# Kernel tuning notes

Measured on AMD Instinct MI355X. Metric: run time of the kernel, lower is better.

Reference implementation:

```python
import jax, jax.numpy as jnp
import numpy as np

NEW_SEQ_LEN = 150  # hard-coded in the original forward


def _interp_one(x, length):
    """PyTorch F.interpolate(mode='linear', align_corners=False) on x[:length].
    x: [T, D] float, length: scalar int. Returns [NEW_SEQ_LEN, D]."""
    lf = length.astype(jnp.float32)
    scale = lf / NEW_SEQ_LEN
    src = (jnp.arange(NEW_SEQ_LEN, dtype=jnp.float32) + 0.5) * scale - 0.5
    src = jnp.maximum(src, 0.0)
    i0 = jnp.floor(src).astype(jnp.int32)
    i0 = jnp.minimum(i0, length - 1)
    i1 = jnp.minimum(i0 + 1, length - 1)
    w = (src - i0.astype(jnp.float32))[:, None]  # [150, 1]
    return x[i0] * (1.0 - w) + x[i1] * w


_interp_batch = jax.vmap(_interp_one)  # ragged per-sample interpolation, fused over batch


def setup_inputs() -> dict:
    key = jax.random.key(0)
    ks = jax.random.split(key, 8)
    B, T, C_IMU, C_EMG, EMB, CSD = 2048, 512, 48, 16, 64, 256
    x_imu = jax.random.normal(ks[0], (B, T, C_IMU), jnp.float32)
    x_emg = jax.random.normal(ks[1], (B, T, C_EMG), jnp.float32)
    lens = jax.random.randint(ks[2], (B,), 160, T + 1, jnp.int32)  # >= NEW_SEQ_LEN
    w_emb_imu = jax.random.normal(ks[3], (C_IMU, EMB), jnp.float32) / np.sqrt(C_IMU)
    b_emb_imu = jnp.zeros((EMB,), jnp.float32)
    w_emb_emg = jax.random.normal(ks[4], (C_EMG, EMB), jnp.float32) / np.sqrt(C_EMG)
    b_emb_emg = jnp.zeros((EMB,), jnp.float32)
    w_proj = jax.random.normal(ks[5], (NEW_SEQ_LEN * EMB, CSD), jnp.float32) / np.sqrt(NEW_SEQ_LEN * EMB)
    b_proj = jnp.zeros((CSD,), jnp.float32)
    return {"x_imu": x_imu, "x_emg": x_emg, "lens": lens,
            "w_emb_imu": w_emb_imu, "b_emb_imu": b_emb_imu,
            "w_emb_emg": w_emb_emg, "b_emb_emg": b_emb_emg,
            "w_proj": w_proj, "b_proj": b_proj}


def reference(x_imu, x_emg, lens, w_emb_imu, b_emb_imu, w_emb_emg, b_emb_emg, w_proj, b_proj):
    B = x_imu.shape[0]
    # embedding nets (per-timestep linear encoders) -> [B, T, 64]
    seq_imu = jnp.einsum('btc,ce->bte', x_imu, w_emb_imu) + b_emb_imu
    seq_emg = jnp.einsum('btc,ce->bte', x_emg, w_emb_emg) + b_emb_emg
    # ragged linear interpolation of each sample's first lens[i] steps to 150
    seq_imu = _interp_batch(seq_imu, lens)  # [B, 150, 64]
    seq_emg = _interp_batch(seq_emg, lens)
    # flatten and project; NOTE: original code applies linear_proj_imu to BOTH
    out_imu = seq_imu.reshape(B, -1) @ w_proj + b_proj
    out_emg = seq_emg.reshape(B, -1) @ w_proj + b_proj
    return (out_imu, out_emg)
```

## Files before the change

### kernel.cpp

```cpp
#include <hip/hip_runtime.h>

#define NEWL 150
#define EMBD 64
#define NCOL 256
#define CIMU 48
#define CEMG 16

#define KIMU (NEWL * CIMU)
#define KEMG (NEWL * CEMG)
#define KSTI 225
#define KSTE 75
#define NCI 5
#define SCH_I 30
#define NG_I 15
#define NG_E 25

typedef __bf16 bf16x8_t __attribute__((ext_vector_type(8)));
typedef __bf16 bf16x4_t __attribute__((ext_vector_type(4)));
typedef float f32x4_t __attribute__((ext_vector_type(4)));

__device__ __forceinline__ f32x4_t mfma16(bf16x8_t a, bf16x8_t b, f32x4_t c) {
  return __builtin_amdgcn_mfma_f32_16x16x32_bf16(a, b, c, 0, 0, 0);
}

template <int C, int KST>
__device__ void wcomb_body(const float* __restrict__ wemb,
                           const float* __restrict__ wreg_src,
                           __bf16* __restrict__ wpk, int s, int j) {
  float wreg[EMBD];
#pragma unroll
  for (int e = 0; e < EMBD; ++e) wreg[e] = wreg_src[(size_t)e * NCOL];
  const int cb = j >> 4, lr = j & 15;
#pragma unroll
  for (int q = 0; q < C / 8; ++q) {
    const int kq = (s * C) / 8 + q;
    const int ks = kq >> 2, h = kq & 3;
    bf16x8_t tv;
#pragma unroll
    for (int u = 0; u < 8; ++u) {
      const float* we = wemb + (q * 8 + u) * EMBD;
      float acc = 0.f;
#pragma unroll
      for (int e = 0; e < EMBD; ++e) acc = fmaf(we[e], wreg[e], acc);
      tv[u] = (__bf16)acc;
    }
    *(bf16x8_t*)(wpk + (((size_t)cb * KST + ks) * 64 + h * 16 + lr) * 8) = tv;
  }
}

__global__ __launch_bounds__(256) void wcomb_kernel(
    const float* __restrict__ w_emb_imu, const float* __restrict__ w_emb_emg,
    const float* __restrict__ b_emb_imu, const float* __restrict__ b_emb_emg,
    const float* __restrict__ w_proj,
    __bf16* __restrict__ wpk_imu, __bf16* __restrict__ wpk_emg,
    float* __restrict__ bpart) {
  const int s = blockIdx.x, m = blockIdx.y, j = threadIdx.x;
  const float* wp_base = w_proj + (size_t)s * EMBD * NCOL + j;
  const float* be = (m == 0) ? b_emb_imu : b_emb_emg;
  float bacc = 0.f;
#pragma unroll
  for (int e = 0; e < EMBD; ++e) bacc = fmaf(be[e], wp_base[(size_t)e * NCOL], bacc);
  bpart[((size_t)m * NEWL + s) * NCOL + j] = bacc;
  if (m == 0)
    wcomb_body<CIMU, KSTI>(w_emb_imu, wp_base, wpk_imu, s, j);
  else
    wcomb_body<CEMG, KSTE>(w_emb_emg, wp_base, wpk_emg, s, j);
}

__global__ __launch_bounds__(256) void fused_kernel(
    const float* __restrict__ x_imu, const float* __restrict__ x_emg,
    const int* __restrict__ lens,
    const __bf16* __restrict__ wpk_imu, const __bf16* __restrict__ wpk_emg,
    const float* __restrict__ b_proj, const float* __restrict__ bpart,
    float* __restrict__ p_imu, float* __restrict__ p_emg,
    float* __restrict__ bias, int B, int T) {
  const int bid = blockIdx.x;
  const int span = B >> 4;
  const int mts = B >> 5;
  if (bid == (NCI + 1) * span) {
    const int j = threadIdx.x;
#pragma unroll
    for (int m = 0; m < 2; ++m) {
      float acc = b_proj[j];
      for (int s = 0; s < NEWL; ++s) acc += bpart[((size_t)m * NEWL + s) * NCOL + j];
      bias[m * NCOL + j] = acc;
    }
    return;
  }

  __shared__ __bf16 lds[2][2][3][512];

  const int tid = threadIdx.x;
  const int wv = tid >> 6, l = tid & 63;

  bool is_imu;
  int c, r;
  if (bid < NCI * span) { is_imu = true; c = bid / span; r = bid - c * span; }
  else { is_imu = false; c = 0; r = bid - NCI * span; }
  const int nh = r / mts, mt = r - nh * mts;

  const __bf16* Wp = is_imu ? wpk_imu : wpk_emg;
  const int KST = is_imu ? KSTI : KSTE;
  const int ks0 = is_imu ? c * 45 : 0;
  const int NG = is_imu ? NG_I : NG_E;
  float* P = is_imu ? (p_imu + (size_t)c * B * NCOL) : p_emg;

  const size_t PS = (size_t)KST * 512;
  const __bf16* bg = Wp + ((size_t)(nh * 8 + wv * 2) * KST + ks0) * 512 + l * 8;

  const int q = tid & 3, sl = (tid >> 2) & 1, bli = tid >> 3;
  const int ble = tid / 6, se = tid - ble * 6;
  const bool act = is_imu || (tid < 192);
  const int b_g = mt * 32 + (is_imu ? bli : ble);
  int lenv = 1;
  float scale = 0.f;
  if (act) { lenv = lens[b_g]; scale = (float)lenv / 150.0f; }
  const int prt_i = (l & ~3) | 2 | (q & 1);

  float gr[2][32];
  float wS[2];
  bf16x8_t bB[2][6];
  f32x4_t acc00 = {0.f, 0.f, 0.f, 0.f}, acc01 = acc00, acc10 = acc00, acc11 = acc00;

#define ISSUE_GI(g2, Pp) do {                                                   \
    const int s_ = c * SCH_I + (g2) * 2 + sl;                                   \
    float src_ = fmaxf(((float)s_ + 0.5f) * scale - 0.5f, 0.0f);                \
    int i0_ = min((int)floorf(src_), lenv - 1);                                 \
    int i1_ = min(i0_ + 1, lenv - 1);                                           \
    wS[Pp] = src_ - (float)i0_;                                                 \
    const float* p_ =                                                           \
        x_imu + ((size_t)b_g * T + ((q < 2) ? i0_ : i1_)) * CIMU + (q & 1) * 24;\
    _Pragma("unroll")                                                           \
    for (int t = 0; t < 6; ++t) {                                               \
      float4 v_ = *(const float4*)(p_ + t * 4);                                 \
      gr[Pp][t * 4 + 0] = v_.x; gr[Pp][t * 4 + 1] = v_.y;                       \
      gr[Pp][t * 4 + 2] = v_.z; gr[Pp][t * 4 + 3] = v_.w;                       \
    }                                                                           \
  } while (0)

#define LERP_WI(Pp, BUF) do {                                                   \
    const float wg_ = wS[Pp], om_ = 1.0f - wg_;                                 \
    _Pragma("unroll")                                                           \
    for (int t = 0; t < 6; ++t) {                                               \
      float a0_ = gr[Pp][t * 4 + 0], a1_ = gr[Pp][t * 4 + 1];                   \
      float a2_ = gr[Pp][t * 4 + 2], a3_ = gr[Pp][t * 4 + 3];                   \
      float p0_ = __shfl(a0_, prt_i), p1_ = __shfl(a1_, prt_i);                 \
      float p2_ = __shfl(a2_, prt_i), p3_ = __shfl(a3_, prt_i);                 \
      if (q < 2) {                                                              \
        bf16x4_t o_;                                                            \
        o_[0] = (__bf16)(a0_ * om_ + p0_ * wg_);                                \
        o_[1] = (__bf16)(a1_ * om_ + p1_ * wg_);                                \
        o_[2] = (__bf16)(a2_ * om_ + p2_ * wg_);                                \
        o_[3] = (__bf16)(a3_ * om_ + p3_ * wg_);                                \
        const int kq_ = sl * 6 + q * 3 + (t >> 1);                              \
        *(bf16x4_t*)(&lds[BUF][bli >> 4][kq_ >> 2]                              \
                         [((kq_ & 3) * 16 + (bli & 15)) * 8 + (t & 1) * 4]) = o_;\
      }                                                                         \
    }                                                                           \
  } while (0)

#define ISSUE_GE(g2, Pp) do { if (tid < 192) {                                  \
    const int s_ = (g2) * 6 + se;                                               \
    float src_ = fmaxf(((float)s_ + 0.5f) * scale - 0.5f, 0.0f);                \
    int i0_ = min((int)floorf(src_), lenv - 1);                                 \
    int i1_ = min(i0_ + 1, lenv - 1);                                           \
    wS[Pp] = src_ - (float)i0_;                                                 \
    const float* p0_ = x_emg + ((size_t)b_g * T + i0_) * CEMG;                  \
    const float* p1_ = x_emg + ((size_t)b_g * T + i1_) * CEMG;                  \
    _Pragma("unroll")                                                           \
    for (int t = 0; t < 4; ++t) {                                               \
      float4 v_ = *(const float4*)(p0_ + t * 4);                                \
      gr[Pp][t * 4 + 0] = v_.x; gr[Pp][t * 4 + 1] = v_.y;                       \
      gr[Pp][t * 4 + 2] = v_.z; gr[Pp][t * 4 + 3] = v_.w;                       \
      float4 u_ = *(const float4*)(p1_ + t * 4);                                \
      gr[Pp][16 + t * 4 + 0] = u_.x; gr[Pp][16 + t * 4 + 1] = u_.y;             \
      gr[Pp][16 + t * 4 + 2] = u_.z; gr[Pp][16 + t * 4 + 3] = u_.w;             \
    }                                                                           \
  } } while (0)

#define LERP_WE(Pp, BUF) do { if (tid < 192) {                                  \
    const float wg_ = wS[Pp], om_ = 1.0f - wg_;                                 \
    _Pragma("unroll")                                                           \
    for (int t2 = 0; t2 < 2; ++t2) {                                            \
      bf16x8_t o_;                                                              \
      _Pragma("unroll")                                                         \
      for (int u = 0; u < 8; ++u)                                               \
        o_[u] = (__bf16)(gr[Pp][t2 * 8 + u] * om_ +                             \
                         gr[Pp][16 + t2 * 8 + u] * wg_);                        \
      const int kq_ = se * 2 + t2;                                              \
      *(bf16x8_t*)(&lds[BUF][ble >> 4][kq_ >> 2]                                \
                       [((kq_ & 3) * 16 + (ble & 15)) * 8]) = o_;               \
    }                                                                           \
  } } while (0)

#define ISSUE_B(g1, Ss) do {                                                    \
    const __bf16* pb_ = bg + (size_t)((g1) * 3) * 512;                          \
    _Pragma("unroll")                                                           \
    for (int ks = 0; ks < 3; ++ks) {                                            \
      bB[Ss][ks * 2 + 0] = *(const bf16x8_t*)(pb_ + (size_t)ks * 512);          \
      bB[Ss][ks * 2 + 1] = *(const bf16x8_t*)(pb_ + PS + (size_t)ks * 512);     \
    }                                                                           \
  } while (0)

#define COMPUTE(Pp) do {                                                        \
    _Pragma("unroll")                                                           \
    for (int ks = 0; ks < 3; ++ks) {                                            \
      bf16x8_t a0_ = *(const bf16x8_t*)(&lds[Pp][0][ks][l * 8]);                \
      bf16x8_t a1_ = *(const bf16x8_t*)(&lds[Pp][1][ks][l * 8]);                \
      acc00 = mfma16(a0_, bB[Pp][ks * 2 + 0], acc00);                           \
      acc01 = mfma16(a0_, bB[Pp][ks * 2 + 1], acc01);                           \
      acc10 = mfma16(a1_, bB[Pp][ks * 2 + 0], acc10);                           \
      acc11 = mfma16(a1_, bB[Pp][ks * 2 + 1], acc11);                           \
    }                                                                           \
  } while (0)

  if (is_imu) { ISSUE_GI(0, 0); ISSUE_GI(1, 1); }
  else        { ISSUE_GE(0, 0); ISSUE_GE(1, 1); }
  ISSUE_B(0, 0);
  if (is_imu) LERP_WI(0, 0); else LERP_WE(0, 0);
  __syncthreads();

  for (int g = 0; g < NG; g += 2) {
    if (g + 2 < NG) { if (is_imu) ISSUE_GI(g + 2, 0); else ISSUE_GE(g + 2, 0); }
    if (g + 1 < NG) ISSUE_B(g + 1, 1);
    COMPUTE(0);
    if (g + 1 < NG) { if (is_imu) LERP_WI(1, 1); else LERP_WE(1, 1); }
    __syncthreads();
    if (g + 1 < NG) {
      if (g + 3 < NG) { if (is_imu) ISSUE_GI(g + 3, 1); else ISSUE_GE(g + 3, 1); }
      if (g + 2 < NG) ISSUE_B(g + 2, 0);
      COMPUTE(1);
      if (g + 2 < NG) { if (is_imu) LERP_WI(0, 0); else LERP_WE(0, 0); }
      __syncthreads();
    }
  }

  const int lh = l >> 4, lr = l & 15;
  float* Pb = P + (size_t)(mt * 32 + lh * 4) * NCOL + nh * 128 + wv * 32 + lr;
#pragma unroll
  for (int jj = 0; jj < 4; ++jj) {
    Pb[(size_t)jj * NCOL] = acc00[jj];
    Pb[(size_t)jj * NCOL + 16] = acc01[jj];
    Pb[(size_t)(16 + jj) * NCOL] = acc10[jj];
    Pb[(size_t)(16 + jj) * NCOL + 16] = acc11[jj];
  }
#undef ISSUE_GI
#undef LERP_WI
#undef ISSUE_GE
#undef LERP_WE
#undef ISSUE_B
#undef COMPUTE
}

__global__ __launch_bounds__(256) void combine_kernel(
    const float* __restrict__ bias, const float* __restrict__ p_imu,
    const float* __restrict__ p_emg, float* __restrict__ out, int B) {
  const int b = blockIdx.x, m = blockIdx.y, j = threadIdx.x;
  const size_t n = (size_t)B * NCOL;
  const size_t o = (size_t)b * NCOL + j;
  if (m == 0) {
    float v = bias[j];
#pragma unroll
    for (int c = 0; c < NCI; ++c) v += p_imu[c * n + o];
    out[o] = v;
  } else {
    out[n + o] = bias[NCOL + j] + p_emg[o];
  }
}

extern "C" void kernel_launch(void* const* d_in, const int* in_sizes, int n_in,
                              void* d_out, int out_size, void* d_ws, size_t ws_size,
                              hipStream_t stream) {
  const float* x_imu     = (const float*)d_in[0];
  const float* x_emg     = (const float*)d_in[1];
  const int*   lens      = (const int*)d_in[2];
  const float* w_emb_imu = (const float*)d_in[3];
  const float* b_emb_imu = (const float*)d_in[4];
  const float* w_emb_emg = (const float*)d_in[5];
  const float* b_emb_emg = (const float*)d_in[6];
  const float* w_proj    = (const float*)d_in[7];
  const float* b_proj    = (const float*)d_in[8];
  float* out = (float*)d_out;

  const int B = in_sizes[2];
  const int T = in_sizes[0] / (B * CIMU);

  char* ws = (char*)d_ws;
  __bf16* wpk_imu = (__bf16*)ws;  ws += (size_t)NCOL * KIMU * 2;
  __bf16* wpk_emg = (__bf16*)ws;  ws += (size_t)NCOL * KEMG * 2;
  float*  bias    = (float*)ws;   ws += 2 * NCOL * 4;
  float*  bpart   = (float*)ws;   ws += (size_t)2 * NEWL * NCOL * 4;
  float*  p_imu   = (float*)ws;   ws += (size_t)NCI * B * NCOL * 4;
  float*  p_emg   = (float*)ws;   ws += (size_t)B * NCOL * 4;

  wcomb_kernel<<<dim3(NEWL, 2), 256, 0, stream>>>(
      w_emb_imu, w_emb_emg, b_emb_imu, b_emb_emg, w_proj, wpk_imu, wpk_emg, bpart);
  const int span = B >> 4;
  const int nblk = (NCI + 1) * span + 1;
  fused_kernel<<<nblk, 256, 0, stream>>>(x_imu, x_emg, lens, wpk_imu, wpk_emg,
                                         b_proj, bpart, p_imu, p_emg, bias, B, T);
  combine_kernel<<<dim3(B, 2), 256, 0, stream>>>(bias, p_imu, p_emg, out, B);
}
```

Before: 95.09 us.

## Fuse EMG bias into GEMM epilogue, merge wcomb modalities, lighten barriers

The EMG GEMM now adds its bias in the epilogue and writes straight to the output, so the p_emg buffer and its pass in combine_kernel go away. Bias reduction moves out of the fused kernel into a separate small kernel. wcomb loads each w_proj column once and builds both modality packs from it. __syncthreads is replaced with an lgkmcnt wait plus s_barrier, and floorf becomes an int cast, which is valid because src is clamped non-negative. The cost is one extra kernel launch.

```diff
diff --git a/kernel.cpp b/kernel.cpp
--- a/kernel.cpp
+++ b/kernel.cpp
@@ -6,8 +6,6 @@
 #define CIMU 48
 #define CEMG 16
 
-#define KIMU (NEWL * CIMU)
-#define KEMG (NEWL * CEMG)
 #define KSTI 225
 #define KSTE 75
 #define NCI 5
@@ -23,13 +21,16 @@
   return __builtin_amdgcn_mfma_f32_16x16x32_bf16(a, b, c, 0, 0, 0);
 }
 
+#define BAR() do {                                          \
+    asm volatile("s_waitcnt lgkmcnt(0)" ::: "memory");      \
+    __builtin_amdgcn_s_barrier();                           \
+    asm volatile("" ::: "memory");                          \
+  } while (0)
+
 template <int C, int KST>
-__device__ void wcomb_body(const float* __restrict__ wemb,
-                           const float* __restrict__ wreg_src,
-                           __bf16* __restrict__ wpk, int s, int j) {
-  float wreg[EMBD];
-#pragma unroll
-  for (int e = 0; e < EMBD; ++e) wreg[e] = wreg_src[(size_t)e * NCOL];
+__device__ __forceinline__ void wcomb_body(const float* __restrict__ wemb,
+                                           const float* wreg,
+                                           __bf16* __restrict__ wpk, int s, int j) {
   const int cb = j >> 4, lr = j & 15;
 #pragma unroll
   for (int q = 0; q < C / 8; ++q) {
@@ -54,42 +55,43 @@
     const float* __restrict__ w_proj,
     __bf16* __restrict__ wpk_imu, __bf16* __restrict__ wpk_emg,
     float* __restrict__ bpart) {
-  const int s = blockIdx.x, m = blockIdx.y, j = threadIdx.x;
+  const int s = blockIdx.x, j = threadIdx.x;
   const float* wp_base = w_proj + (size_t)s * EMBD * NCOL + j;
-  const float* be = (m == 0) ? b_emb_imu : b_emb_emg;
-  float bacc = 0.f;
-#pragma unroll
-  for (int e = 0; e < EMBD; ++e) bacc = fmaf(be[e], wp_base[(size_t)e * NCOL], bacc);
-  bpart[((size_t)m * NEWL + s) * NCOL + j] = bacc;
-  if (m == 0)
-    wcomb_body<CIMU, KSTI>(w_emb_imu, wp_base, wpk_imu, s, j);
-  else
-    wcomb_body<CEMG, KSTE>(w_emb_emg, wp_base, wpk_emg, s, j);
+  float wreg[EMBD];
+#pragma unroll
+  for (int e = 0; e < EMBD; ++e) wreg[e] = wp_base[(size_t)e * NCOL];
+  float bi = 0.f, be = 0.f;
+#pragma unroll
+  for (int e = 0; e < EMBD; ++e) {
+    bi = fmaf(b_emb_imu[e], wreg[e], bi);
+    be = fmaf(b_emb_emg[e], wreg[e], be);
+  }
+  bpart[(size_t)s * NCOL + j] = bi;
+  bpart[((size_t)NEWL + s) * NCOL + j] = be;
+  wcomb_body<CIMU, KSTI>(w_emb_imu, wreg, wpk_imu, s, j);
+  wcomb_body<CEMG, KSTE>(w_emb_emg, wreg, wpk_emg, s, j);
+}
+
+__global__ __launch_bounds__(256) void bias_kernel(
+    const float* __restrict__ b_proj, const float* __restrict__ bpart,
+    float* __restrict__ bias) {
+  const int m = blockIdx.x, j = threadIdx.x;
+  float acc = b_proj[j];
+  for (int s = 0; s < NEWL; ++s) acc += bpart[((size_t)m * NEWL + s) * NCOL + j];
+  bias[m * NCOL + j] = acc;
 }
 
 __global__ __launch_bounds__(256) void fused_kernel(
     const float* __restrict__ x_imu, const float* __restrict__ x_emg,
     const int* __restrict__ lens,
     const __bf16* __restrict__ wpk_imu, const __bf16* __restrict__ wpk_emg,
-    const float* __restrict__ b_proj, const float* __restrict__ bpart,
-    float* __restrict__ p_imu, float* __restrict__ p_emg,
-    float* __restrict__ bias, int B, int T) {
+    const float* __restrict__ bias, float* __restrict__ p_imu,
+    float* __restrict__ out, int B, int T) {
+  __shared__ __bf16 lds[2][2][3][512];
+
   const int bid = blockIdx.x;
   const int span = B >> 4;
   const int mts = B >> 5;
-  if (bid == (NCI + 1) * span) {
-    const int j = threadIdx.x;
-#pragma unroll
-    for (int m = 0; m < 2; ++m) {
-      float acc = b_proj[j];
-      for (int s = 0; s < NEWL; ++s) acc += bpart[((size_t)m * NEWL + s) * NCOL + j];
-      bias[m * NCOL + j] = acc;
-    }
-    return;
-  }
-
-  __shared__ __bf16 lds[2][2][3][512];
-
   const int tid = threadIdx.x;
   const int wv = tid >> 6, l = tid & 63;
 
@@ -103,18 +105,18 @@
   const int KST = is_imu ? KSTI : KSTE;
   const int ks0 = is_imu ? c * 45 : 0;
   const int NG = is_imu ? NG_I : NG_E;
-  float* P = is_imu ? (p_imu + (size_t)c * B * NCOL) : p_emg;
+  float* P = is_imu ? (p_imu + (size_t)c * B * NCOL) : (out + (size_t)B * NCOL);
 
   const size_t PS = (size_t)KST * 512;
   const __bf16* bg = Wp + ((size_t)(nh * 8 + wv * 2) * KST + ks0) * 512 + l * 8;
 
   const int q = tid & 3, sl = (tid >> 2) & 1, bli = tid >> 3;
-  const int ble = tid / 6, se = tid - ble * 6;
+  const int ble = tid / 6, se = tid - (tid / 6) * 6;
   const bool act = is_imu || (tid < 192);
-  const int b_g = mt * 32 + (is_imu ? bli : ble);
+  const int b_g = mt * 32 + (is_imu ? bli : (act ? ble : 0));
   int lenv = 1;
   float scale = 0.f;
-  if (act) { lenv = lens[b_g]; scale = (float)lenv / 150.0f; }
+  if (act) { lenv = lens[b_g]; scale = (float)lenv * (1.0f / 150.0f); }
   const int prt_i = (l & ~3) | 2 | (q & 1);
 
   float gr[2][32];
@@ -125,7 +127,7 @@
 #define ISSUE_GI(g2, Pp) do {                                                   \
     const int s_ = c * SCH_I + (g2) * 2 + sl;                                   \
     float src_ = fmaxf(((float)s_ + 0.5f) * scale - 0.5f, 0.0f);                \
-    int i0_ = min((int)floorf(src_), lenv - 1);                                 \
+    int i0_ = min((int)src_, lenv - 1);                                         \
     int i1_ = min(i0_ + 1, lenv - 1);                                           \
     wS[Pp] = src_ - (float)i0_;                                                 \
     const float* p_ =                                                           \
@@ -159,10 +161,10 @@
     }                                                                           \
   } while (0)
 
-#define ISSUE_GE(g2, Pp) do { if (tid < 192) {                                  \
+#define ISSUE_GE(g2, Pp) do { if (act) {                                        \
     const int s_ = (g2) * 6 + se;                                               \
     float src_ = fmaxf(((float)s_ + 0.5f) * scale - 0.5f, 0.0f);                \
-    int i0_ = min((int)floorf(src_), lenv - 1);                                 \
+    int i0_ = min((int)src_, lenv - 1);                                         \
     int i1_ = min(i0_ + 1, lenv - 1);                                           \
     wS[Pp] = src_ - (float)i0_;                                                 \
     const float* p0_ = x_emg + ((size_t)b_g * T + i0_) * CEMG;                  \
@@ -178,7 +180,7 @@
     }                                                                           \
   } } while (0)
 
-#define LERP_WE(Pp, BUF) do { if (tid < 192) {                                  \
+#define LERP_WE(Pp, BUF) do { if (act) {                                        \
     const float wg_ = wS[Pp], om_ = 1.0f - wg_;                                 \
     _Pragma("unroll")                                                           \
     for (int t2 = 0; t2 < 2; ++t2) {                                            \
@@ -218,31 +220,41 @@
   else        { ISSUE_GE(0, 0); ISSUE_GE(1, 1); }
   ISSUE_B(0, 0);
   if (is_imu) LERP_WI(0, 0); else LERP_WE(0, 0);
-  __syncthreads();
-
-  for (int g = 0; g < NG; g += 2) {
-    if (g + 2 < NG) { if (is_imu) ISSUE_GI(g + 2, 0); else ISSUE_GE(g + 2, 0); }
-    if (g + 1 < NG) ISSUE_B(g + 1, 1);
-    COMPUTE(0);
-    if (g + 1 < NG) { if (is_imu) LERP_WI(1, 1); else LERP_WE(1, 1); }
-    __syncthreads();
+  BAR();
+
+  for (int gp = 0; gp < (NG_E + 1) / 2; ++gp) {
+    const int g = gp * 2;
+    if (g >= NG) break;
+    {
+      if (g + 2 < NG) { if (is_imu) ISSUE_GI(g + 2, 0); else ISSUE_GE(g + 2, 0); }
+      if (g + 1 < NG) ISSUE_B(g + 1, 1);
+      COMPUTE(0);
+      if (g + 1 < NG) { if (is_imu) LERP_WI(1, 1); else LERP_WE(1, 1); }
+      BAR();
+    }
     if (g + 1 < NG) {
       if (g + 3 < NG) { if (is_imu) ISSUE_GI(g + 3, 1); else ISSUE_GE(g + 3, 1); }
       if (g + 2 < NG) ISSUE_B(g + 2, 0);
       COMPUTE(1);
       if (g + 2 < NG) { if (is_imu) LERP_WI(0, 0); else LERP_WE(0, 0); }
-      __syncthreads();
+      BAR();
     }
   }
 
   const int lh = l >> 4, lr = l & 15;
-  float* Pb = P + (size_t)(mt * 32 + lh * 4) * NCOL + nh * 128 + wv * 32 + lr;
+  const int colb = nh * 128 + wv * 32;
+  float b0 = 0.f, b1 = 0.f;
+  if (!is_imu) {
+    b0 = bias[NCOL + colb + lr];
+    b1 = bias[NCOL + colb + 16 + lr];
+  }
+  float* Pb = P + (size_t)(mt * 32 + lh * 4) * NCOL + colb + lr;
 #pragma unroll
   for (int jj = 0; jj < 4; ++jj) {
-    Pb[(size_t)jj * NCOL] = acc00[jj];
-    Pb[(size_t)jj * NCOL + 16] = acc01[jj];
-    Pb[(size_t)(16 + jj) * NCOL] = acc10[jj];
-    Pb[(size_t)(16 + jj) * NCOL + 16] = acc11[jj];
+    Pb[(size_t)jj * NCOL] = acc00[jj] + b0;
+    Pb[(size_t)jj * NCOL + 16] = acc01[jj] + b1;
+    Pb[(size_t)(16 + jj) * NCOL] = acc10[jj] + b0;
+    Pb[(size_t)(16 + jj) * NCOL + 16] = acc11[jj] + b1;
   }
 #undef ISSUE_GI
 #undef LERP_WI
@@ -254,18 +266,14 @@
 
 __global__ __launch_bounds__(256) void combine_kernel(
     const float* __restrict__ bias, const float* __restrict__ p_imu,
-    const float* __restrict__ p_emg, float* __restrict__ out, int B) {
-  const int b = blockIdx.x, m = blockIdx.y, j = threadIdx.x;
+    float* __restrict__ out, int B) {
+  const int b = blockIdx.x, j = threadIdx.x;
   const size_t n = (size_t)B * NCOL;
   const size_t o = (size_t)b * NCOL + j;
-  if (m == 0) {
-    float v = bias[j];
-#pragma unroll
-    for (int c = 0; c < NCI; ++c) v += p_imu[c * n + o];
-    out[o] = v;
-  } else {
-    out[n + o] = bias[NCOL + j] + p_emg[o];
-  }
+  float v = bias[j];
+#pragma unroll
+  for (int c = 0; c < NCI; ++c) v += p_imu[c * n + o];
+  out[o] = v;
 }
 
 extern "C" void kernel_launch(void* const* d_in, const int* in_sizes, int n_in,
@@ -286,18 +294,18 @@
   const int T = in_sizes[0] / (B * CIMU);
 
   char* ws = (char*)d_ws;
-  __bf16* wpk_imu = (__bf16*)ws;  ws += (size_t)NCOL * KIMU * 2;
-  __bf16* wpk_emg = (__bf16*)ws;  ws += (size_t)NCOL * KEMG * 2;
+  __bf16* wpk_imu = (__bf16*)ws;  ws += (size_t)NCOL * KSTI * 32 * 2;
+  __bf16* wpk_emg = (__bf16*)ws;  ws += (size_t)NCOL * KSTE * 32 * 2;
   float*  bias    = (float*)ws;   ws += 2 * NCOL * 4;
   float*  bpart   = (float*)ws;   ws += (size_t)2 * NEWL * NCOL * 4;
   float*  p_imu   = (float*)ws;   ws += (size_t)NCI * B * NCOL * 4;
-  float*  p_emg   = (float*)ws;   ws += (size_t)B * NCOL * 4;
-
-  wcomb_kernel<<<dim3(NEWL, 2), 256, 0, stream>>>(
-      w_emb_imu, w_emb_emg, b_emb_imu, b_emb_emg, w_proj, wpk_imu, wpk_emg, bpart);
-  const int span = B >> 4;
-  const int nblk = (NCI + 1) * span + 1;
+
+  wcomb_kernel<<<NEWL, 256, 0, stream>>>(w_emb_imu, w_emb_emg, b_emb_imu,
+                                         b_emb_emg, w_proj, wpk_imu, wpk_emg,
+                                         bpart);
+  bias_kernel<<<2, 256, 0, stream>>>(b_proj, bpart, bias);
+  const int nblk = (NCI + 1) * (B >> 4);
   fused_kernel<<<nblk, 256, 0, stream>>>(x_imu, x_emg, lens, wpk_imu, wpk_emg,
-                                         b_proj, bpart, p_imu, p_emg, bias, B, T);
-  combine_kernel<<<dim3(B, 2), 256, 0, stream>>>(bias, p_imu, p_emg, out, B);
-}
+                                         bias, p_imu, out, B, T);
+  combine_kernel<<<B, 256, 0, stream>>>(bias, p_imu, out, B);
+}
```

New measurement: 113.6 us. 1.19x slower.
